# Optimization experiments

Measured on AMD Instinct MI355X. Metric: run time of the kernel, lower is better.

Reference implementation:

```python
import jax, jax.numpy as jnp
import numpy as np

NUM_BLOCKS, NUM_LAYERS = 3, 10
DILATIONS = tuple(2 ** l for l in range(NUM_LAYERS)) * NUM_BLOCKS  # 30 layers
B, T = 2, 8192
MEL_C, RES_C, SKIP_C, K = 80, 512, 256, 3


def conv1d(x, w, b, dilation=1):
    # x: (B, Cin, T), w: (Cout, Cin, K), 'same' padding = dilation*(K-1)//2
    pad = dilation * (w.shape[-1] - 1) // 2
    y = jax.lax.conv_general_dilated(
        x, w, window_strides=(1,), padding=[(pad, pad)],
        rhs_dilation=(dilation,), dimension_numbers=("NCH", "OIH", "NCH"))
    return y + b[None, :, None]


def setup_inputs() -> dict:
    key = jax.random.key(0)
    ks = jax.random.split(key, 16)
    s = 0.05  # keep activations in a sane range through the gated stack
    return {
        "mel_spec": jax.random.normal(ks[0], (B, MEL_C, T), jnp.float32),
        "audio":    jax.random.normal(ks[1], (B, 1, T), jnp.float32),
        "start_w":  jax.random.normal(ks[2], (RES_C, 1, 1), jnp.float32) * s,
        "start_b":  jax.random.normal(ks[3], (RES_C,), jnp.float32) * s,
        "mel_w":    jax.random.normal(ks[4], (RES_C, MEL_C, 1), jnp.float32) * s,
        "mel_b":    jax.random.normal(ks[5], (RES_C,), jnp.float32) * s,
        "dil_w":    jax.random.normal(ks[6], (30, 2 * RES_C, RES_C, K), jnp.float32) * s,
        "dil_b":    jax.random.normal(ks[7], (30, 2 * RES_C), jnp.float32) * s,
        "res_w":    jax.random.normal(ks[8], (30, RES_C, RES_C, 1), jnp.float32) * s,
        "res_b":    jax.random.normal(ks[9], (30, RES_C), jnp.float32) * s,
        "skip_w":   jax.random.normal(ks[10], (30, SKIP_C, RES_C, 1), jnp.float32) * s,
        "skip_b":   jax.random.normal(ks[11], (30, SKIP_C), jnp.float32) * s,
        "fc1_w":    jax.random.normal(ks[12], (SKIP_C, SKIP_C, 1), jnp.float32) * s,
        "fc1_b":    jax.random.normal(ks[13], (SKIP_C,), jnp.float32) * s,
        "fc2_w":    jax.random.normal(ks[14], (1, SKIP_C, 1), jnp.float32) * s,
        "fc2_b":    jax.random.normal(ks[15], (1,), jnp.float32) * s,
    }


def reference(mel_spec, audio, start_w, start_b, mel_w, mel_b,
              dil_w, dil_b, res_w, res_b, skip_w, skip_b,
              fc1_w, fc1_b, fc2_w, fc2_b):
    x = conv1d(audio, start_w, start_b)                 # (B, RES_C, T)
    mel_cond = conv1d(mel_spec, mel_w, mel_b)           # (B, RES_C, T) -- same length, no interp
    x = x + mel_cond
    skip_sum = jnp.zeros((x.shape[0], SKIP_C, x.shape[2]), x.dtype)
    for i, d in enumerate(DILATIONS):                   # 30 structurally distinct layers
        h = conv1d(x, dil_w[i], dil_b[i], dilation=d)   # (B, 2*RES_C, T)
        f, g = jnp.split(h, 2, axis=1)
        a = jnp.tanh(f) * jax.nn.sigmoid(g)             # gated activation
        x = x + conv1d(a, res_w[i], res_b[i])
        skip_sum = skip_sum + conv1d(a, skip_w[i], skip_b[i])
    y = jax.nn.relu(conv1d(skip_sum, fc1_w, fc1_b))
    return jnp.tanh(conv1d(y, fc2_w, fc2_b))            # (B, 1, T)
```

## Files before the change

### kernel.cpp

```cpp
#include <hip/hip_runtime.h>
#include <stdint.h>

#define TB 8192
#define NBATCH 2
#define RES_C 512
#define SKIP_C 256
#define MEL_C 80
#define NLAYERS 30

typedef short v8s __attribute__((ext_vector_type(8)));
typedef float v4f __attribute__((ext_vector_type(4)));
typedef unsigned short v4u16 __attribute__((ext_vector_type(4)));
typedef unsigned short v8u16 __attribute__((ext_vector_type(8)));

__device__ __forceinline__ unsigned short bf16rne(float f) {
    unsigned u = __float_as_uint(f);
    return (unsigned short)((u + 0x7fffu + ((u >> 16) & 1u)) >> 16);
}
__device__ __forceinline__ float bf2f(unsigned short h) {
    return __uint_as_float((unsigned)h << 16);
}
__device__ __forceinline__ float fsigmoid(float x) { return 1.0f / (1.0f + __expf(-x)); }
__device__ __forceinline__ float ftanh_(float x) { return 2.0f / (1.0f + __expf(-2.0f * x)) - 1.0f; }

__device__ __forceinline__ void gld16(const void* g, void* l) {
    __builtin_amdgcn_global_load_lds(
        (const __attribute__((address_space(1))) unsigned int*)g,
        (__attribute__((address_space(3))) unsigned int*)l, 16, 0, 0);
}

__global__ void k0_pack(const float* __restrict__ dil_w,
                        const float* __restrict__ res_w,
                        const float* __restrict__ skip_w,
                        unsigned short* __restrict__ Wp,
                        unsigned short* __restrict__ Wq,
                        int split)
{
    const int TC = split + 1;
    const int NWp = NLAYERS << 16;
    const int NWq = NLAYERS * 49152;
    const int total = NWp + NWq;
    const int stride = gridDim.x * blockDim.x;
    for (int i = blockIdx.x * blockDim.x + threadIdx.x; i < total; i += stride) {
        if (i < NWp) {
            const int l15 = i & 15;
            const int quad = (i >> 4) & 3;
            const int kc = (i >> 6) & 3;
            const int ks = (i >> 8) & 3;
            const int mt = (i >> 10) & 1;
            const int fg = (i >> 11) & 1;
            const int wv = (i >> 12) & 7;
            const int p = (i >> 15) & 1;
            const int l = i >> 16;
            const int co = fg * 512 + p * 256 + wv * 32 + mt * 16 + l15;
            const int ci0 = ks * 128 + kc * 32 + quad * 8;
            const int lane = quad * 16 + l15;
            const float* src = dil_w + ((size_t)(l * 1024 + co) * 512 + ci0) * 3;
            float buf[24];
            #pragma unroll
            for (int q = 0; q < 6; ++q) {
                v4f v = *(const v4f*)(src + q * 4);
                buf[q * 4 + 0] = v[0]; buf[q * 4 + 1] = v[1];
                buf[q * 4 + 2] = v[2]; buf[q * 4 + 3] = v[3];
            }
            unsigned short* lbase = Wp + (size_t)l * 3072 * TC * 512 + lane * 8;
            #pragma unroll
            for (int tap = 0; tap < 3; ++tap) {
                v8u16 hi, lo;
                #pragma unroll
                for (int e = 0; e < 8; ++e) {
                    const float w = buf[e * 3 + tap];
                    const unsigned short h = bf16rne(w);
                    hi[e] = h;
                    lo[e] = bf16rne(w - bf2f(h));
                }
                const int idx = ((p * 8 + wv) * 192
                               + ((tap * 4 + ks) * 16 + kc * 4 + mt * 2 + fg)) * TC;
                unsigned short* d = lbase + (size_t)idx * 512;
                *(v8u16*)d = hi;
                if (split) *(v8u16*)(d + 512) = lo;
            }
        } else {
            const int j = i - NWp;
            const int l = j / 49152;
            const int r = j - l * 49152;
            const int l15 = r & 15;
            const int quad = (r >> 4) & 3;
            const int kc = (r >> 6) & 15;
            const int rowgrp = r >> 10;
            const int rowc = rowgrp * 16 + l15;
            const int ci0 = kc * 32 + quad * 8;
            const int lane = quad * 16 + l15;
            const int wv = rowgrp / 6, i6 = rowgrp % 6;
            const float* src = (rowc < 512)
                ? res_w + ((size_t)(l * 512 + rowc) * 512 + ci0)
                : skip_w + ((size_t)(l * 256 + (rowc - 512)) * 512 + ci0);
            v4f v0 = *(const v4f*)(src);
            v4f v1 = *(const v4f*)(src + 4);
            float buf[8] = {v0[0], v0[1], v0[2], v0[3], v1[0], v1[1], v1[2], v1[3]};
            v8u16 hi, lo;
            #pragma unroll
            for (int e = 0; e < 8; ++e) {
                const float w = buf[e];
                const unsigned short h = bf16rne(w);
                hi[e] = h;
                lo[e] = bf16rne(w - bf2f(h));
            }
            const int idx = (wv * 96 + kc * 6 + i6) * TC;
            unsigned short* d = Wq + (size_t)l * 768 * TC * 512 + (size_t)idx * 512
                              + lane * 8;
            *(v8u16*)d = hi;
            if (split) *(v8u16*)(d + 512) = lo;
        }
    }
}

__global__ __launch_bounds__(512)
void k_init(const float* __restrict__ audio, const float* __restrict__ mel,
            const float* __restrict__ start_w, const float* __restrict__ start_b,
            const float* __restrict__ mel_w, const float* __restrict__ mel_b,
            float* __restrict__ x0,
            unsigned short* __restrict__ xH, unsigned short* __restrict__ xL,
            float* __restrict__ skip_acc, int split)
{
    __shared__ float smel[MEL_C][64];
    __shared__ float sa[64];
    const int tid = threadIdx.x;
    const int b = blockIdx.x >> 7;
    const int t0 = (blockIdx.x & 127) << 6;
    for (int i = tid; i < MEL_C * 64; i += 512) {
        const int m = i >> 6, tt = i & 63;
        smel[m][tt] = mel[((size_t)b * MEL_C + m) * TB + t0 + tt];
    }
    if (tid < 64) sa[tid] = audio[(size_t)b * TB + t0 + tid];
    for (int i = tid; i < 64 * SKIP_C; i += 512) {
        const int tt = i >> 8, c = i & 255;
        skip_acc[(size_t)(b * TB + t0 + tt) * SKIP_C + c] = 0.f;
    }
    __syncthreads();
    const int c = tid;
    const float sw = start_w[c];
    const float bias = start_b[c] + mel_b[c];
    const float* wrow = mel_w + (size_t)c * MEL_C;
    v4f acc[16];
    #pragma unroll
    for (int q = 0; q < 16; ++q) {
        v4f av = *(const v4f*)&sa[q * 4];
        acc[q][0] = fmaf(sw, av[0], bias);
        acc[q][1] = fmaf(sw, av[1], bias);
        acc[q][2] = fmaf(sw, av[2], bias);
        acc[q][3] = fmaf(sw, av[3], bias);
    }
    for (int m = 0; m < MEL_C; ++m) {
        const float w = wrow[m];
        #pragma unroll
        for (int q = 0; q < 16; ++q) {
            v4f mv = *(const v4f*)&smel[m][q * 4];
            acc[q][0] = fmaf(w, mv[0], acc[q][0]);
            acc[q][1] = fmaf(w, mv[1], acc[q][1]);
            acc[q][2] = fmaf(w, mv[2], acc[q][2]);
            acc[q][3] = fmaf(w, mv[3], acc[q][3]);
        }
    }
    #pragma unroll
    for (int q = 0; q < 16; ++q) {
        #pragma unroll
        for (int e = 0; e < 4; ++e) {
            const int tt = q * 4 + e;
            const size_t o = (size_t)(b * TB + t0 + tt) * RES_C + c;
            const float v = acc[q][e];
            x0[o] = v;
            const unsigned short h = bf16rne(v);
            xH[o] = h;
            if (split) xL[o] = bf16rne(v - bf2f(h));
        }
    }
}

__global__ __launch_bounds__(512)
void k1_dilgate(const unsigned short* __restrict__ xH,
                const unsigned short* __restrict__ xL,
                unsigned short* __restrict__ aH, unsigned short* __restrict__ aL,
                const unsigned short* __restrict__ Wp,
                const float* __restrict__ dil_b,
                int dil, int split)
{
    __shared__ unsigned short shb2[2][128 * 128];
    __shared__ unsigned short slb2[2][128 * 128];
    const int TC = split + 1;
    const int tid = threadIdx.x;
    const int wave = tid >> 6, lane = tid & 63;
    const int quad = lane >> 4, l15 = lane & 15;
    const int p = blockIdx.x & 1;
    const int tl = blockIdx.x >> 1;
    const int b = tl >> 6;
    const int t0 = (tl & 63) << 7;
    const int srow = lane >> 4;
    const int schunk = lane & 15;
    const unsigned short* wpw = Wp + ((size_t)(p * 8 + wave) * 192 * TC) * 512 + lane * 8;

    const v4f vz = {0.f, 0.f, 0.f, 0.f};
    v4f accF[2][8], accG[2][8];
    #pragma unroll
    for (int mt = 0; mt < 2; ++mt)
        #pragma unroll
        for (int n = 0; n < 8; ++n) { accF[mt][n] = vz; accG[mt][n] = vz; }

    auto stage = [&](int chunk, int buf) {
        const int tap = chunk >> 2, ks = chunk & 3;
        const int off = (tap - 1) * dil;
        const bool allok = (t0 + off >= 0) && (t0 + 127 + off < TB);
        unsigned short* dsth = shb2[buf];
        unsigned short* dstl = slb2[buf];
        if (allok) {
            #pragma unroll
            for (int q = 0; q < 4; ++q) {
                const int rbase = wave * 16 + q * 4;
                const int r = rbase + srow;
                const size_t go = (size_t)(b * TB + t0 + r + off) * RES_C
                                + ks * 128 + ((schunk ^ (r & 7)) << 3);
                gld16(xH + go, dsth + rbase * 128);
                if (split) gld16(xL + go, dstl + rbase * 128);
            }
        } else {
            #pragma unroll
            for (int q = 0; q < 4; ++q) {
                const int rbase = wave * 16 + q * 4;
                const int r = rbase + srow;
                const int tsrc = t0 + r + off;
                const bool ok = (unsigned)tsrc < TB;
                const size_t go = (size_t)(b * TB + tsrc) * RES_C
                                + ks * 128 + ((schunk ^ (r & 7)) << 3);
                v8u16 vh = ok ? *(const v8u16*)(xH + go) : (v8u16)0;
                *(v8u16*)(dsth + rbase * 128 + (lane << 3)) = vh;
                if (split) {
                    v8u16 vl = ok ? *(const v8u16*)(xL + go) : (v8u16)0;
                    *(v8u16*)(dstl + rbase * 128 + (lane << 3)) = vl;
                }
            }
        }
    };

    auto compute = [&](int chunk, int buf) {
        const int tap = chunk >> 2, ks = chunk & 3;
        const unsigned short* cb = wpw + (size_t)((tap * 4 + ks) * 16) * TC * 512;
        const unsigned short* shb = shb2[buf];
        const unsigned short* slb = slb2[buf];
        #pragma unroll
        for (int kc = 0; kc < 4; ++kc) {
            const unsigned short* ck = cb + (size_t)(kc * 4) * TC * 512;
            v8s afh[2], agh[2], afl[2], agl[2];
            #pragma unroll
            for (int mt = 0; mt < 2; ++mt) {
                afh[mt] = *(const v8s*)(ck + (size_t)((mt * 2 + 0) * TC) * 512);
                agh[mt] = *(const v8s*)(ck + (size_t)((mt * 2 + 1) * TC) * 512);
                if (split) {
                    afl[mt] = *(const v8s*)(ck + (size_t)((mt * 2 + 0) * TC + 1) * 512);
                    agl[mt] = *(const v8s*)(ck + (size_t)((mt * 2 + 1) * TC + 1) * 512);
                }
            }
            const int nsw = ((kc * 4 + quad) ^ (l15 & 7)) << 3;
            #pragma unroll
            for (int nh = 0; nh < 2; ++nh) {
                v8s bh[4], bl[4];
                #pragma unroll
                for (int j = 0; j < 4; ++j) {
                    const int trow = (nh * 4 + j) * 16 + l15;
                    bh[j] = *(const v8s*)(shb + trow * 128 + nsw);
                    if (split) bl[j] = *(const v8s*)(slb + trow * 128 + nsw);
                }
                #pragma unroll
                for (int mt = 0; mt < 2; ++mt)
                    #pragma unroll
                    for (int j = 0; j < 4; ++j) {
                        const int n = nh * 4 + j;
                        accF[mt][n] = __builtin_amdgcn_mfma_f32_16x16x32_bf16(
                            afh[mt], bh[j], accF[mt][n], 0, 0, 0);
                        accG[mt][n] = __builtin_amdgcn_mfma_f32_16x16x32_bf16(
                            agh[mt], bh[j], accG[mt][n], 0, 0, 0);
                        if (split) {
                            accF[mt][n] = __builtin_amdgcn_mfma_f32_16x16x32_bf16(
                                afh[mt], bl[j], accF[mt][n], 0, 0, 0);
                            accF[mt][n] = __builtin_amdgcn_mfma_f32_16x16x32_bf16(
                                afl[mt], bh[j], accF[mt][n], 0, 0, 0);
                            accG[mt][n] = __builtin_amdgcn_mfma_f32_16x16x32_bf16(
                                agh[mt], bl[j], accG[mt][n], 0, 0, 0);
                            accG[mt][n] = __builtin_amdgcn_mfma_f32_16x16x32_bf16(
                                agl[mt], bh[j], accG[mt][n], 0, 0, 0);
                        }
                    }
            }
        }
    };

    stage(0, 0);
    __syncthreads();
    for (int chunk = 0; chunk < 12; ++chunk) {
        if (chunk < 11) stage(chunk + 1, (chunk + 1) & 1);
        compute(chunk, chunk & 1);
        __syncthreads();
    }

    unsigned short* aHb = aH + (size_t)b * TB * RES_C;
    unsigned short* aLb = aL + (size_t)b * TB * RES_C;
    #pragma unroll
    for (int mt = 0; mt < 2; ++mt) {
        const int ch = p * 256 + wave * 32 + mt * 16 + quad * 4;
        const float4 bF = *(const float4*)(dil_b + ch);
        const float4 bG = *(const float4*)(dil_b + 512 + ch);
        #pragma unroll
        for (int n = 0; n < 8; ++n) {
            const int t = t0 + n * 16 + l15;
            float a0 = ftanh_(accF[mt][n][0] + bF.x) * fsigmoid(accG[mt][n][0] + bG.x);
            float a1 = ftanh_(accF[mt][n][1] + bF.y) * fsigmoid(accG[mt][n][1] + bG.y);
            float a2 = ftanh_(accF[mt][n][2] + bF.z) * fsigmoid(accG[mt][n][2] + bG.z);
            float a3 = ftanh_(accF[mt][n][3] + bF.w) * fsigmoid(accG[mt][n][3] + bG.w);
            v4u16 oh;
            oh[0] = bf16rne(a0); oh[1] = bf16rne(a1);
            oh[2] = bf16rne(a2); oh[3] = bf16rne(a3);
            *(v4u16*)(aHb + (size_t)t * RES_C + ch) = oh;
            if (split) {
                v4u16 ol;
                ol[0] = bf16rne(a0 - bf2f(oh[0]));
                ol[1] = bf16rne(a1 - bf2f(oh[1]));
                ol[2] = bf16rne(a2 - bf2f(oh[2]));
                ol[3] = bf16rne(a3 - bf2f(oh[3]));
                *(v4u16*)(aLb + (size_t)t * RES_C + ch) = ol;
            }
        }
    }
}

__global__ __launch_bounds__(512)
void k3_resskip(float* __restrict__ x,
                unsigned short* __restrict__ xH, unsigned short* __restrict__ xL,
                float* __restrict__ skip_acc,
                const unsigned short* __restrict__ aH,
                const unsigned short* __restrict__ aL,
                const unsigned short* __restrict__ Wq,
                const float* __restrict__ res_b, const float* __restrict__ skip_b,
                int split)
{
    __shared__ unsigned short shi[32 * 512];
    __shared__ unsigned short slo[32 * 512];
    const int TC = split + 1;
    const int tid = threadIdx.x;
    const int wave = tid >> 6, lane = tid & 63;
    const int quad = lane >> 4, l15 = lane & 15;
    const int b = blockIdx.x >> 8;
    const int t0 = (blockIdx.x & 255) << 5;
    const unsigned short* wqw = Wq + (size_t)wave * 96 * TC * 512 + lane * 8;
    {
        #pragma unroll
        for (int q = 0; q < 4; ++q) {
            const int r = wave * 4 + q;
            const size_t go = (size_t)(b * TB + t0 + r) * RES_C + ((lane ^ (r & 7)) << 3);
            gld16(aH + go, shi + r * 512);
            if (split) gld16(aL + go, slo + r * 512);
        }
    }
    __syncthreads();
    const v4f vz = {0.f, 0.f, 0.f, 0.f};
    v4f acc[6][2];
    #pragma unroll
    for (int i = 0; i < 6; ++i) { acc[i][0] = vz; acc[i][1] = vz; }

    for (int kc = 0; kc < 16; ++kc) {
        const int nsw = ((kc * 4 + quad) ^ (l15 & 7)) << 3;
        v8s bh[2], bl[2];
        #pragma unroll
        for (int j = 0; j < 2; ++j) {
            bh[j] = *(const v8s*)(shi + (j * 16 + l15) * 512 + nsw);
            if (split) bl[j] = *(const v8s*)(slo + (j * 16 + l15) * 512 + nsw);
        }
        #pragma unroll
        for (int i = 0; i < 6; ++i) {
            const unsigned short* ck = wqw + (size_t)((kc * 6 + i) * TC) * 512;
            v8s ah, al;
            ah = *(const v8s*)(ck);
            if (split) al = *(const v8s*)(ck + 512);
            #pragma unroll
            for (int j = 0; j < 2; ++j) {
                acc[i][j] = __builtin_amdgcn_mfma_f32_16x16x32_bf16(ah, bh[j], acc[i][j], 0, 0, 0);
                if (split) {
                    acc[i][j] = __builtin_amdgcn_mfma_f32_16x16x32_bf16(ah, bl[j], acc[i][j], 0, 0, 0);
                    acc[i][j] = __builtin_amdgcn_mfma_f32_16x16x32_bf16(al, bh[j], acc[i][j], 0, 0, 0);
                }
            }
        }
    }
    #pragma unroll
    for (int i = 0; i < 6; ++i) {
        const int rb = (wave * 6 + i) * 16 + quad * 4;
        if (rb < 512) {
            const float4 bias = *(const float4*)(res_b + rb);
            #pragma unroll
            for (int j = 0; j < 2; ++j) {
                const int t = t0 + j * 16 + l15;
                const size_t o = (size_t)(b * TB + t) * RES_C + rb;
                float4 v = *(const float4*)(x + o);
                v.x += acc[i][j][0] + bias.x;
                v.y += acc[i][j][1] + bias.y;
                v.z += acc[i][j][2] + bias.z;
                v.w += acc[i][j][3] + bias.w;
                *(float4*)(x + o) = v;
                v4u16 oh;
                oh[0] = bf16rne(v.x); oh[1] = bf16rne(v.y);
                oh[2] = bf16rne(v.z); oh[3] = bf16rne(v.w);
                *(v4u16*)(xH + o) = oh;
                if (split) {
                    v4u16 ol;
                    ol[0] = bf16rne(v.x - bf2f(oh[0]));
                    ol[1] = bf16rne(v.y - bf2f(oh[1]));
                    ol[2] = bf16rne(v.z - bf2f(oh[2]));
                    ol[3] = bf16rne(v.w - bf2f(oh[3]));
                    *(v4u16*)(xL + o) = ol;
                }
            }
        } else {
            const int rs = rb - 512;
            const float4 bias = *(const float4*)(skip_b + rs);
            #pragma unroll
            for (int j = 0; j < 2; ++j) {
                const int t = t0 + j * 16 + l15;
                const size_t o = (size_t)(b * TB + t) * SKIP_C + rs;
                float4 v = *(const float4*)(skip_acc + o);
                v.x += acc[i][j][0] + bias.x;
                v.y += acc[i][j][1] + bias.y;
                v.z += acc[i][j][2] + bias.z;
                v.w += acc[i][j][3] + bias.w;
                *(float4*)(skip_acc + o) = v;
            }
        }
    }
}

__global__ __launch_bounds__(256)
void k4_final(const float* __restrict__ skip_acc,
              const float* __restrict__ fc1_w, const float* __restrict__ fc1_b,
              const float* __restrict__ fc2_w, const float* __restrict__ fc2_b,
              float* __restrict__ out)
{
    __shared__ float stile[32 * 260];
    __shared__ float part[8][32];
    const int tid = threadIdx.x;
    const int b = blockIdx.x >> 8;
    const int t0 = (blockIdx.x & 255) << 5;
    {
        const int r = tid >> 3, sub = tid & 7;
        const float* srow = skip_acc + (size_t)(b * TB + t0 + r) * SKIP_C;
        float* drow = stile + r * 260;
        #pragma unroll
        for (int i = 0; i < 8; ++i) {
            const int c = (i * 8 + sub) * 4;
            *(float4*)(drow + c) = *(const float4*)(srow + c);
        }
    }
    __syncthreads();
    const int t = tid & 31;
    const int w = tid >> 5;
    float y[32];
    #pragma unroll
    for (int co = 0; co < 32; ++co) y[co] = fc1_b[w * 32 + co];
    const float* srow = stile + t * 260;
    for (int ci = 0; ci < SKIP_C; ++ci) {
        const float s = srow[ci];
        const float* wcol = fc1_w + (size_t)(w * 32) * SKIP_C + ci;
        #pragma unroll
        for (int co = 0; co < 32; ++co)
            y[co] = fmaf(wcol[(size_t)co * SKIP_C], s, y[co]);
    }
    float partial = 0.f;
    #pragma unroll
    for (int co = 0; co < 32; ++co) {
        const float v = y[co] > 0.f ? y[co] : 0.f;
        partial = fmaf(fc2_w[w * 32 + co], v, partial);
    }
    part[w][t] = partial;
    __syncthreads();
    if (tid < 32) {
        float v = fc2_b[0];
        #pragma unroll
        for (int k = 0; k < 8; ++k) v += part[k][tid];
        out[(size_t)b * TB + t0 + tid] = ftanh_(v);
    }
}

extern "C" void kernel_launch(void* const* d_in, const int* in_sizes, int n_in,
                              void* d_out, int out_size, void* d_ws, size_t ws_size,
                              hipStream_t stream)
{
    const float* mel     = (const float*)d_in[0];
    const float* audio   = (const float*)d_in[1];
    const float* start_w = (const float*)d_in[2];
    const float* start_b = (const float*)d_in[3];
    const float* mel_w   = (const float*)d_in[4];
    const float* mel_b   = (const float*)d_in[5];
    const float* dil_b   = (const float*)d_in[7];
    const float* res_b   = (const float*)d_in[9];
    const float* skip_b  = (const float*)d_in[11];
    const float* fc1_w   = (const float*)d_in[12];
    const float* fc1_b   = (const float*)d_in[13];
    const float* fc2_w   = (const float*)d_in[14];
    const float* fc2_b   = (const float*)d_in[15];
    float* out = (float*)d_out;

    char* ws = (char*)d_ws;
    const size_t szX32 = (size_t)NBATCH * TB * RES_C * 4;
    const size_t szX16 = (size_t)NBATCH * TB * RES_C * 2;
    const size_t szSk = (size_t)NBATCH * TB * SKIP_C * 4;
    const size_t need2 = (size_t)NLAYERS * 3072 * 2 * 512 * 2
                       + (size_t)NLAYERS * 768 * 2 * 512 * 2
                       + szX32 + szSk + 4 * szX16;
    const int split = (ws_size >= need2) ? 1 : 0;
    const int TC = split + 1;
    const size_t szWp = (size_t)NLAYERS * 3072 * TC * 512 * 2;
    const size_t szWq = (size_t)NLAYERS * 768 * TC * 512 * 2;
    size_t off = 0;
    unsigned short* Wp = (unsigned short*)(ws + off); off += szWp;
    unsigned short* Wq = (unsigned short*)(ws + off); off += szWq;
    float* x = (float*)(ws + off); off += szX32;
    unsigned short* xH = (unsigned short*)(ws + off); off += szX16;
    unsigned short* aH = (unsigned short*)(ws + off); off += szX16;
    float* skip_acc = (float*)(ws + off); off += szSk;
    unsigned short* xL = split ? (unsigned short*)(ws + off) : xH; if (split) off += szX16;
    unsigned short* aL = split ? (unsigned short*)(ws + off) : aH; if (split) off += szX16;

    k0_pack<<<8192, 256, 0, stream>>>((const float*)d_in[6], (const float*)d_in[8],
                                      (const float*)d_in[10], Wp, Wq, split);
    k_init<<<NBATCH * (TB / 64), 512, 0, stream>>>(
        audio, mel, start_w, start_b, mel_w, mel_b, x, xH, xL, skip_acc, split);

    for (int l = 0; l < NLAYERS; ++l) {
        const int dil = 1 << (l % 10);
        k1_dilgate<<<256, 512, 0, stream>>>(xH, xL, aH, aL,
            Wp + (size_t)l * 3072 * TC * 512,
            dil_b + (size_t)l * 1024, dil, split);
        k3_resskip<<<512, 512, 0, stream>>>(x, xH, xL, skip_acc, aH, aL,
            Wq + (size_t)l * 768 * TC * 512,
            res_b + (size_t)l * 512, skip_b + (size_t)l * 256, split);
    }
    k4_final<<<512, 256, 0, stream>>>(skip_acc, fc1_w, fc1_b, fc2_w, fc2_b, out);
}
```

Measured before the change: 6.946 ms.

## Retile dilated-gate kernel to 64-step blocks with 4 waves and repacked weights

The dilated conv + gate kernel now uses 256-thread blocks that each cover 64 time steps and 128 filter channels, launched as 1024 blocks instead of 256. The K loop is split into 24 chunks of 64 input channels, and the weight packing in the pack kernel is reordered to match. The aim is to fill more of the CUs than the old 256-block grid did and to raise occupancy through smaller LDS tiles and a launch-bounds hint of 3 blocks. In exchange, each block reuses less data, so every x tile is reloaded by four channel-group blocks, and there are twice as many barrier-separated chunks.

```diff
diff --git a/kernel.cpp b/kernel.cpp
--- a/kernel.cpp
+++ b/kernel.cpp
@@ -45,23 +45,23 @@
         if (i < NWp) {
             const int l15 = i & 15;
             const int quad = (i >> 4) & 3;
-            const int kc = (i >> 6) & 3;
-            const int ks = (i >> 8) & 3;
+            const int kc = (i >> 6) & 1;
+            const int ks8 = (i >> 7) & 7;
             const int mt = (i >> 10) & 1;
             const int fg = (i >> 11) & 1;
-            const int wv = (i >> 12) & 7;
-            const int p = (i >> 15) & 1;
+            const int w = (i >> 12) & 3;
+            const int q = (i >> 14) & 3;
             const int l = i >> 16;
-            const int co = fg * 512 + p * 256 + wv * 32 + mt * 16 + l15;
-            const int ci0 = ks * 128 + kc * 32 + quad * 8;
+            const int co = fg * 512 + q * 128 + w * 32 + mt * 16 + l15;
+            const int ci0 = ks8 * 64 + kc * 32 + quad * 8;
             const int lane = quad * 16 + l15;
             const float* src = dil_w + ((size_t)(l * 1024 + co) * 512 + ci0) * 3;
             float buf[24];
             #pragma unroll
-            for (int q = 0; q < 6; ++q) {
-                v4f v = *(const v4f*)(src + q * 4);
-                buf[q * 4 + 0] = v[0]; buf[q * 4 + 1] = v[1];
-                buf[q * 4 + 2] = v[2]; buf[q * 4 + 3] = v[3];
+            for (int v = 0; v < 6; ++v) {
+                v4f x = *(const v4f*)(src + v * 4);
+                buf[v * 4 + 0] = x[0]; buf[v * 4 + 1] = x[1];
+                buf[v * 4 + 2] = x[2]; buf[v * 4 + 3] = x[3];
             }
             unsigned short* lbase = Wp + (size_t)l * 3072 * TC * 512 + lane * 8;
             #pragma unroll
@@ -69,14 +69,14 @@
                 v8u16 hi, lo;
                 #pragma unroll
                 for (int e = 0; e < 8; ++e) {
-                    const float w = buf[e * 3 + tap];
-                    const unsigned short h = bf16rne(w);
+                    const float wv = buf[e * 3 + tap];
+                    const unsigned short h = bf16rne(wv);
                     hi[e] = h;
-                    lo[e] = bf16rne(w - bf2f(h));
+                    lo[e] = bf16rne(wv - bf2f(h));
                 }
-                const int idx = ((p * 8 + wv) * 192
-                               + ((tap * 4 + ks) * 16 + kc * 4 + mt * 2 + fg)) * TC;
-                unsigned short* d = lbase + (size_t)idx * 512;
+                const int g = (q * 4 + w) * 192
+                            + (((tap * 8 + ks8) * 2 + kc) * 4 + mt * 2 + fg);
+                unsigned short* d = lbase + (size_t)(g * TC) * 512;
                 *(v8u16*)d = hi;
                 if (split) *(v8u16*)(d + 512) = lo;
             }
@@ -101,10 +101,10 @@
             v8u16 hi, lo;
             #pragma unroll
             for (int e = 0; e < 8; ++e) {
-                const float w = buf[e];
-                const unsigned short h = bf16rne(w);
+                const float wt = buf[e];
+                const unsigned short h = bf16rne(wt);
                 hi[e] = h;
-                lo[e] = bf16rne(w - bf2f(h));
+                lo[e] = bf16rne(wt - bf2f(h));
             }
             const int idx = (wv * 96 + kc * 6 + i6) * TC;
             unsigned short* d = Wq + (size_t)l * 768 * TC * 512 + (size_t)idx * 512
@@ -177,7 +177,7 @@
     }
 }
 
-__global__ __launch_bounds__(512)
+__global__ __launch_bounds__(256, 3)
 void k1_dilgate(const unsigned short* __restrict__ xH,
                 const unsigned short* __restrict__ xL,
                 unsigned short* __restrict__ aH, unsigned short* __restrict__ aL,
@@ -185,118 +185,118 @@
                 const float* __restrict__ dil_b,
                 int dil, int split)
 {
-    __shared__ unsigned short shb2[2][128 * 128];
-    __shared__ unsigned short slb2[2][128 * 128];
+    __shared__ unsigned short shb2[2][64 * 64];
+    __shared__ unsigned short slb2[2][64 * 64];
     const int TC = split + 1;
     const int tid = threadIdx.x;
     const int wave = tid >> 6, lane = tid & 63;
     const int quad = lane >> 4, l15 = lane & 15;
-    const int p = blockIdx.x & 1;
-    const int tl = blockIdx.x >> 1;
-    const int b = tl >> 6;
-    const int t0 = (tl & 63) << 7;
-    const int srow = lane >> 4;
-    const int schunk = lane & 15;
-    const unsigned short* wpw = Wp + ((size_t)(p * 8 + wave) * 192 * TC) * 512 + lane * 8;
+    const int idx = blockIdx.x;
+    const int tpar = idx & 1;
+    const int q = (idx >> 1) & 3;
+    const int j6 = (idx >> 3) & 63;
+    const int b = idx >> 9;
+    const int t0 = (j6 * 2 + tpar) << 6;
+    const int fbase = q * 128 + wave * 32;
+    const unsigned short* wpw = Wp + ((size_t)(q * 4 + wave) * 192 * TC) * 512 + lane * 8;
 
     const v4f vz = {0.f, 0.f, 0.f, 0.f};
-    v4f accF[2][8], accG[2][8];
+    v4f accF[2][4], accG[2][4];
     #pragma unroll
     for (int mt = 0; mt < 2; ++mt)
         #pragma unroll
-        for (int n = 0; n < 8; ++n) { accF[mt][n] = vz; accG[mt][n] = vz; }
+        for (int n = 0; n < 4; ++n) { accF[mt][n] = vz; accG[mt][n] = vz; }
 
     auto stage = [&](int chunk, int buf) {
-        const int tap = chunk >> 2, ks = chunk & 3;
+        const int tap = chunk >> 3, ks8 = chunk & 7;
         const int off = (tap - 1) * dil;
-        const bool allok = (t0 + off >= 0) && (t0 + 127 + off < TB);
+        const bool allok = (t0 + off >= 0) && (t0 + 63 + off < TB);
         unsigned short* dsth = shb2[buf];
         unsigned short* dstl = slb2[buf];
+        const int rl = lane >> 3;
+        const int c = lane & 7;
         if (allok) {
             #pragma unroll
-            for (int q = 0; q < 4; ++q) {
-                const int rbase = wave * 16 + q * 4;
-                const int r = rbase + srow;
+            for (int i = 0; i < 2; ++i) {
+                const int rbase = wave * 16 + i * 8;
+                const int r = rbase + rl;
+                const int cs = c ^ (r & 7);
                 const size_t go = (size_t)(b * TB + t0 + r + off) * RES_C
-                                + ks * 128 + ((schunk ^ (r & 7)) << 3);
-                gld16(xH + go, dsth + rbase * 128);
-                if (split) gld16(xL + go, dstl + rbase * 128);
+                                + ks8 * 64 + cs * 8;
+                gld16(xH + go, dsth + rbase * 64);
+                if (split) gld16(xL + go, dstl + rbase * 64);
             }
         } else {
             #pragma unroll
-            for (int q = 0; q < 4; ++q) {
-                const int rbase = wave * 16 + q * 4;
-                const int r = rbase + srow;
+            for (int i = 0; i < 2; ++i) {
+                const int rbase = wave * 16 + i * 8;
+                const int r = rbase + rl;
                 const int tsrc = t0 + r + off;
                 const bool ok = (unsigned)tsrc < TB;
-                const size_t go = (size_t)(b * TB + tsrc) * RES_C
-                                + ks * 128 + ((schunk ^ (r & 7)) << 3);
+                const int cs = c ^ (r & 7);
+                const size_t go = (size_t)(b * TB + tsrc) * RES_C + ks8 * 64 + cs * 8;
                 v8u16 vh = ok ? *(const v8u16*)(xH + go) : (v8u16)0;
-                *(v8u16*)(dsth + rbase * 128 + (lane << 3)) = vh;
+                *(v8u16*)(dsth + rbase * 64 + lane * 8) = vh;
                 if (split) {
                     v8u16 vl = ok ? *(const v8u16*)(xL + go) : (v8u16)0;
-                    *(v8u16*)(dstl + rbase * 128 + (lane << 3)) = vl;
+                    *(v8u16*)(dstl + rbase * 64 + lane * 8) = vl;
                 }
             }
         }
     };
 
     auto compute = [&](int chunk, int buf) {
-        const int tap = chunk >> 2, ks = chunk & 3;
-        const unsigned short* cb = wpw + (size_t)((tap * 4 + ks) * 16) * TC * 512;
+        const int tap = chunk >> 3, ks8 = chunk & 7;
+        const unsigned short* cb = wpw + (size_t)((tap * 8 + ks8) * 8) * TC * 512;
         const unsigned short* shb = shb2[buf];
         const unsigned short* slb = slb2[buf];
         #pragma unroll
-        for (int kc = 0; kc < 4; ++kc) {
-            const unsigned short* ck = cb + (size_t)(kc * 4) * TC * 512;
+        for (int kc = 0; kc < 2; ++kc) {
+            const unsigned short* ck = cb + (size_t)(kc * 4 * TC) * 512;
             v8s afh[2], agh[2], afl[2], agl[2];
             #pragma unroll
             for (int mt = 0; mt < 2; ++mt) {
                 afh[mt] = *(const v8s*)(ck + (size_t)((mt * 2 + 0) * TC) * 512);
                 agh[mt] = *(const v8s*)(ck + (size_t)((mt * 2 + 1) * TC) * 512);
                 if (split) {
-                    afl[mt] = *(const v8s*)(ck + (size_t)((mt * 2 + 0) * TC + 1) * 512);
-                    agl[mt] = *(const v8s*)(ck + (size_t)((mt * 2 + 1) * TC + 1) * 512);
+                    afl[mt] = *(const v8s*)(ck + (size_t)((mt * 2 + 0) * TC) * 512 + 512);
+                    agl[mt] = *(const v8s*)(ck + (size_t)((mt * 2 + 1) * TC) * 512 + 512);
                 }
             }
             const int nsw = ((kc * 4 + quad) ^ (l15 & 7)) << 3;
-            #pragma unroll
-            for (int nh = 0; nh < 2; ++nh) {
-                v8s bh[4], bl[4];
+            v8s bh[4], bl[4];
+            #pragma unroll
+            for (int j = 0; j < 4; ++j) {
+                const int trow = j * 16 + l15;
+                bh[j] = *(const v8s*)(shb + trow * 64 + nsw);
+                if (split) bl[j] = *(const v8s*)(slb + trow * 64 + nsw);
+            }
+            #pragma unroll
+            for (int mt = 0; mt < 2; ++mt)
                 #pragma unroll
                 for (int j = 0; j < 4; ++j) {
-                    const int trow = (nh * 4 + j) * 16 + l15;
-                    bh[j] = *(const v8s*)(shb + trow * 128 + nsw);
-                    if (split) bl[j] = *(const v8s*)(slb + trow * 128 + nsw);
+                    accF[mt][j] = __builtin_amdgcn_mfma_f32_16x16x32_bf16(
+                        afh[mt], bh[j], accF[mt][j], 0, 0, 0);
+                    accG[mt][j] = __builtin_amdgcn_mfma_f32_16x16x32_bf16(
+                        agh[mt], bh[j], accG[mt][j], 0, 0, 0);
+                    if (split) {
+                        accF[mt][j] = __builtin_amdgcn_mfma_f32_16x16x32_bf16(
+                            afh[mt], bl[j], accF[mt][j], 0, 0, 0);
+                        accF[mt][j] = __builtin_amdgcn_mfma_f32_16x16x32_bf16(
+                            afl[mt], bh[j], accF[mt][j], 0, 0, 0);
+                        accG[mt][j] = __builtin_amdgcn_mfma_f32_16x16x32_bf16(
+                            agh[mt], bl[j], accG[mt][j], 0, 0, 0);
+                        accG[mt][j] = __builtin_amdgcn_mfma_f32_16x16x32_bf16(
+                            agl[mt], bh[j], accG[mt][j], 0, 0, 0);
+                    }
                 }
-                #pragma unroll
-                for (int mt = 0; mt < 2; ++mt)
-                    #pragma unroll
-                    for (int j = 0; j < 4; ++j) {
-                        const int n = nh * 4 + j;
-                        accF[mt][n] = __builtin_amdgcn_mfma_f32_16x16x32_bf16(
-                            afh[mt], bh[j], accF[mt][n], 0, 0, 0);
-                        accG[mt][n] = __builtin_amdgcn_mfma_f32_16x16x32_bf16(
-                            agh[mt], bh[j], accG[mt][n], 0, 0, 0);
-                        if (split) {
-                            accF[mt][n] = __builtin_amdgcn_mfma_f32_16x16x32_bf16(
-                                afh[mt], bl[j], accF[mt][n], 0, 0, 0);
-                            accF[mt][n] = __builtin_amdgcn_mfma_f32_16x16x32_bf16(
-                                afl[mt], bh[j], accF[mt][n], 0, 0, 0);
-                            accG[mt][n] = __builtin_amdgcn_mfma_f32_16x16x32_bf16(
-                                agh[mt], bl[j], accG[mt][n], 0, 0, 0);
-                            accG[mt][n] = __builtin_amdgcn_mfma_f32_16x16x32_bf16(
-                                agl[mt], bh[j], accG[mt][n], 0, 0, 0);
-                        }
-                    }
-            }
         }
     };
 
     stage(0, 0);
     __syncthreads();
-    for (int chunk = 0; chunk < 12; ++chunk) {
-        if (chunk < 11) stage(chunk + 1, (chunk + 1) & 1);
+    for (int chunk = 0; chunk < 24; ++chunk) {
+        if (chunk < 23) stage(chunk + 1, (chunk + 1) & 1);
         compute(chunk, chunk & 1);
         __syncthreads();
     }
@@ -305,11 +305,11 @@
     unsigned short* aLb = aL + (size_t)b * TB * RES_C;
     #pragma unroll
     for (int mt = 0; mt < 2; ++mt) {
-        const int ch = p * 256 + wave * 32 + mt * 16 + quad * 4;
+        const int ch = fbase + mt * 16 + quad * 4;
         const float4 bF = *(const float4*)(dil_b + ch);
         const float4 bG = *(const float4*)(dil_b + 512 + ch);
         #pragma unroll
-        for (int n = 0; n < 8; ++n) {
+        for (int n = 0; n < 4; ++n) {
             const int t = t0 + n * 16 + l15;
             float a0 = ftanh_(accF[mt][n][0] + bF.x) * fsigmoid(accG[mt][n][0] + bG.x);
             float a1 = ftanh_(accF[mt][n][1] + bF.y) * fsigmoid(accG[mt][n][1] + bG.y);
@@ -533,7 +533,7 @@
 
     for (int l = 0; l < NLAYERS; ++l) {
         const int dil = 1 << (l % 10);
-        k1_dilgate<<<256, 512, 0, stream>>>(xH, xL, aH, aL,
+        k1_dilgate<<<1024, 256, 0, stream>>>(xH, xL, aH, aL,
             Wp + (size_t)l * 3072 * TC * 512,
             dil_b + (size_t)l * 1024, dil, split);
         k3_resskip<<<512, 512, 0, stream>>>(x, xH, xL, skip_acc, aH, aL,
```

Measured after the change: 7.123 ms. 1.03x slower.
